# Kernel tuning notes

Measured on AMD Instinct MI355X. Metric: run time of the kernel, lower is better.

## Reference

```python
import jax, jax.numpy as jnp
import numpy as np

N_USER, N_ITEM = 100000, 50000
E = 500000
D, ED = 128, 16


def setup_inputs() -> dict:
    key = jax.random.key(0)
    ks = jax.random.split(key, 14)
    return {
        "h_user": jax.random.normal(ks[0], (N_USER, D), jnp.float32),
        "h_item": jax.random.normal(ks[1], (N_ITEM, D), jnp.float32),
        "ef_orders": jax.random.normal(ks[2], (E, ED), jnp.float32),
        "ef_rev": jax.random.normal(ks[3], (E, ED), jnp.float32),
        "W1": jax.random.normal(ks[4], (2 * D + ED, 128), jnp.float32) * 0.05,
        "b1": jax.random.normal(ks[5], (128,), jnp.float32) * 0.05,
        "W2": jax.random.normal(ks[6], (128, 32), jnp.float32) * 0.05,
        "b2": jax.random.normal(ks[7], (32,), jnp.float32) * 0.05,
        "W3": jax.random.normal(ks[8], (32, 1), jnp.float32) * 0.05,
        "b3": jax.random.normal(ks[9], (1,), jnp.float32) * 0.05,
        "src_orders": jax.random.randint(ks[10], (E,), 0, N_USER, jnp.int64),
        "dst_orders": jax.random.randint(ks[11], (E,), 0, N_ITEM, jnp.int64),
        "src_rev": jax.random.randint(ks[12], (E,), 0, N_ITEM, jnp.int64),
        "dst_rev": jax.random.randint(ks[13], (E,), 0, N_USER, jnp.int64),
    }


def _edge_mlp(h_src, h_dst, src, dst, ef, W1, b1, W2, b2, W3, b3):
    # gather per-edge endpoint embeddings, concat with edge features: [E, 2D+ED]
    x = jnp.concatenate([h_src[src], h_dst[dst], ef], axis=1)
    x = jax.nn.relu(x @ W1 + b1)   # [E, 128]
    x = jax.nn.relu(x @ W2 + b2)   # [E, 32]
    return jax.nn.sigmoid(x @ W3 + b3)  # [E, 1]


def reference(h_user, h_item, ef_orders, ef_rev, W1, b1, W2, b2, W3, b3,
              src_orders, dst_orders, src_rev, dst_rev):
    # etype (user, orders, item)
    out_orders = _edge_mlp(h_user, h_item, src_orders, dst_orders, ef_orders,
                           W1, b1, W2, b2, W3, b3)
    # etype (item, rev-orders, user)
    out_rev = _edge_mlp(h_item, h_user, src_rev, dst_rev, ef_rev,
                        W1, b1, W2, b2, W3, b3)
    return out_orders, out_rev
```

## Files before the change

kernel.cpp:

```cpp
#include <hip/hip_runtime.h>
#include <hip/hip_bf16.h>

typedef __attribute__((ext_vector_type(8))) short bfrag;
typedef __attribute__((ext_vector_type(4))) float facc;
typedef __attribute__((ext_vector_type(2))) float f32x2;

static __device__ __forceinline__ float bf2f_lo(unsigned int u) {
    return __uint_as_float(u << 16);
}
static __device__ __forceinline__ float bf2f_hi(unsigned int u) {
    return __uint_as_float(u & 0xffff0000u);
}
static __device__ __forceinline__ unsigned short f2bf(float f) {
    __hip_bfloat16 b = __float2bfloat16(f);
    return *reinterpret_cast<unsigned short*>(&b);
}

extern "C" __global__ __launch_bounds__(256)
void precompute_mfma(const float* __restrict__ hu, int nu,
                     const float* __restrict__ hi, int ni,
                     const float* __restrict__ W1,
                     unsigned char* __restrict__ Yu,
                     unsigned char* __restrict__ Yi)
{
    const int tid = threadIdx.x, wave = tid >> 6, lane = tid & 63;
    const int g = lane >> 4, e16 = lane & 15;
    const int c0 = wave * 64;

    bfrag bfr[4][4];
    #pragma unroll
    for (int nt = 0; nt < 4; ++nt) {
        const int j = c0 + nt * 16 + e16;
        #pragma unroll
        for (int kk = 0; kk < 4; ++kk) {
            bfrag v;
            #pragma unroll
            for (int i = 0; i < 8; ++i) {
                int k = kk * 32 + g * 8 + i;
                float w = (j < 128) ? W1[(size_t)k * 128 + j]
                                    : W1[(size_t)(128 + k) * 128 + (j - 128)];
                v[i] = (short)f2bf(w);
            }
            bfr[nt][kk] = v;
        }
    }

    const int tu = (nu + 15) >> 4, ti = (ni + 15) >> 4, tt = tu + ti;
    for (int tile = blockIdx.x; tile < tt; tile += gridDim.x) {
        const float* h; unsigned char* Y; int n, node0;
        if (tile < tu) { h = hu; Y = Yu; n = nu; node0 = tile * 16; }
        else           { h = hi; Y = Yi; n = ni; node0 = (tile - tu) * 16; }

        int arow = node0 + e16; if (arow >= n) arow = n - 1;
        facc acc[4] = {{0,0,0,0},{0,0,0,0},{0,0,0,0},{0,0,0,0}};
        #pragma unroll
        for (int kk = 0; kk < 4; ++kk) {
            const float* ap = h + (size_t)arow * 128 + kk * 32 + g * 8;
            float4 a0 = *(const float4*)ap;
            float4 a1v = *(const float4*)(ap + 4);
            bfrag af;
            af[0] = (short)f2bf(a0.x);  af[1] = (short)f2bf(a0.y);
            af[2] = (short)f2bf(a0.z);  af[3] = (short)f2bf(a0.w);
            af[4] = (short)f2bf(a1v.x); af[5] = (short)f2bf(a1v.y);
            af[6] = (short)f2bf(a1v.z); af[7] = (short)f2bf(a1v.w);
            #pragma unroll
            for (int nt = 0; nt < 4; ++nt)
                acc[nt] = __builtin_amdgcn_mfma_f32_16x16x32_bf16(af, bfr[nt][kk], acc[nt], 0, 0, 0);
        }
        #pragma unroll
        for (int nt = 0; nt < 4; ++nt) {
            unsigned int pk = __builtin_amdgcn_cvt_pk_fp8_f32(acc[nt][0], acc[nt][1], 0u, false);
            pk = __builtin_amdgcn_cvt_pk_fp8_f32(acc[nt][2], acc[nt][3], pk, true);
            #pragma unroll
            for (int r = 0; r < 4; ++r) {
                int row = node0 + g * 4 + r;
                if (row < n)
                    Y[(size_t)row * 256 + c0 + nt * 16 + e16] =
                        (unsigned char)(pk >> (8 * r));
            }
        }
    }
}

extern "C" __global__ __launch_bounds__(256, 3)
void edge_mfma(const unsigned char* __restrict__ Yu,
               const unsigned char* __restrict__ Yi,
               const float* __restrict__ ef_orders,
               const float* __restrict__ ef_rev,
               const int* __restrict__ src_orders,
               const int* __restrict__ dst_orders,
               const int* __restrict__ src_rev,
               const int* __restrict__ dst_rev,
               const float* __restrict__ W1,
               const float* __restrict__ b1,
               const float* __restrict__ W2,
               const float* __restrict__ b2,
               const float* __restrict__ W3,
               const float* __restrict__ b3,
               float* __restrict__ out, int E)
{
    __shared__ __align__(16) unsigned short d1_lds[4][16][128];
    const int tid = threadIdx.x, wave = tid >> 6, lane = tid & 63;
    const int g = lane >> 4, e16 = lane & 15;
    unsigned short (*my_lds)[128] = d1_lds[wave];
    const int swzb = (e16 & 7) << 3;

    bfrag a1[8];
    #pragma unroll
    for (int t = 0; t < 8; ++t) {
        bfrag v;
        #pragma unroll
        for (int i = 0; i < 8; ++i) {
            unsigned short s16 = 0;
            if (i < 4)                s16 = f2bf(W1[(size_t)(256 + 4 * g + i) * 128 + t * 16 + e16]);
            else if (i == 4 && g == 0) s16 = f2bf(b1[t * 16 + e16]);
            v[i] = (short)s16;
        }
        a1[t] = v;
    }
    bfrag w2t[2][4];
    #pragma unroll
    for (int nt = 0; nt < 2; ++nt)
        #pragma unroll
        for (int kk = 0; kk < 4; ++kk) {
            bfrag v;
            #pragma unroll
            for (int i = 0; i < 8; ++i) {
                int k = (kk >> 1) * 64 + 16 * g + (kk & 1) * 8 + i;
                v[i] = (short)f2bf(W2[(size_t)k * 32 + nt * 16 + e16]);
            }
            w2t[nt][kk] = v;
        }
    float b2v[2][4], w3v[2][4];
    #pragma unroll
    for (int nt = 0; nt < 2; ++nt)
        #pragma unroll
        for (int r = 0; r < 4; ++r) {
            b2v[nt][r] = b2[nt * 16 + g * 4 + r];
            w3v[nt][r] = W3[nt * 16 + g * 4 + r];
        }
    const float b3s = b3[0];

    const long twoE = 2L * E;
    const int nbatch = (int)((twoE + 15) >> 4);
    const int stride = gridDim.x * 4;
    int b = blockIdx.x * 4 + wave;

    int s_pf = 0, d_pf = 0;
    uint4 ysA, ysB, ydA, ydB;
    float4 efq = make_float4(0, 0, 0, 0);

#define LOADIDX(BB) do {                                                      \
        long el_ = ((long)(BB) << 4) + e16;                                   \
        if (el_ >= twoE) el_ = twoE - 1;                                      \
        const bool rv_ = el_ >= E;                                            \
        const int ee_ = (int)(rv_ ? el_ - E : el_);                           \
        s_pf = (rv_ ? src_rev : src_orders)[ee_];                             \
        d_pf = (rv_ ? dst_rev : dst_orders)[ee_];                             \
    } while (0)

#define GATHER(BB) do {                                                       \
        long el_ = ((long)(BB) << 4) + e16;                                   \
        if (el_ >= twoE) el_ = twoE - 1;                                      \
        const bool rv_ = el_ >= E;                                            \
        const int ee_ = (int)(rv_ ? el_ - E : el_);                           \
        const unsigned char* ps_ = (rv_ ? Yi : Yu) + (size_t)s_pf * 256 + g * 16; \
        const unsigned char* pd_ = (rv_ ? Yu : Yi) + (size_t)d_pf * 256 + 128 + g * 16; \
        ysA = *(const uint4*)(ps_);       ysB = *(const uint4*)(ps_ + 64);    \
        ydA = *(const uint4*)(pd_);       ydB = *(const uint4*)(pd_ + 64);    \
        efq = *(const float4*)((rv_ ? ef_rev : ef_orders) + (size_t)ee_ * 16 + g * 4); \
    } while (0)

#define PSTEP(KK, YSL, YSH, YDL, YDH) do {                                    \
        const int dlo_ = (((KK) >> 1) * 64 + 16 * g + ((KK) & 1) * 8) ^ swzb; \
        uint4 wv = *(const uint4*)&my_lds[e16][dlo_];                         \
        f32x2 s01 = __builtin_amdgcn_cvt_pk_f32_fp8(YSL, false);              \
        f32x2 s23 = __builtin_amdgcn_cvt_pk_f32_fp8(YSL, true);               \
        f32x2 s45 = __builtin_amdgcn_cvt_pk_f32_fp8(YSH, false);              \
        f32x2 s67 = __builtin_amdgcn_cvt_pk_f32_fp8(YSH, true);               \
        f32x2 d01 = __builtin_amdgcn_cvt_pk_f32_fp8(YDL, false);              \
        f32x2 d23 = __builtin_amdgcn_cvt_pk_f32_fp8(YDL, true);               \
        f32x2 d45 = __builtin_amdgcn_cvt_pk_f32_fp8(YDH, false);              \
        f32x2 d67 = __builtin_amdgcn_cvt_pk_f32_fp8(YDH, true);               \
        float p0 = s01[0] + d01[0] + bf2f_lo(wv.x);                           \
        float p1 = s01[1] + d01[1] + bf2f_hi(wv.x);                           \
        float p2 = s23[0] + d23[0] + bf2f_lo(wv.y);                           \
        float p3 = s23[1] + d23[1] + bf2f_hi(wv.y);                           \
        float p4 = s45[0] + d45[0] + bf2f_lo(wv.z);                           \
        float p5 = s45[1] + d45[1] + bf2f_hi(wv.z);                           \
        float p6 = s67[0] + d67[0] + bf2f_lo(wv.w);                           \
        float p7 = s67[1] + d67[1] + bf2f_hi(wv.w);                           \
        bfrag pa;                                                             \
        pa[0] = (short)f2bf(fmaxf(p0, 0.f)); pa[1] = (short)f2bf(fmaxf(p1, 0.f)); \
        pa[2] = (short)f2bf(fmaxf(p2, 0.f)); pa[3] = (short)f2bf(fmaxf(p3, 0.f)); \
        pa[4] = (short)f2bf(fmaxf(p4, 0.f)); pa[5] = (short)f2bf(fmaxf(p5, 0.f)); \
        pa[6] = (short)f2bf(fmaxf(p6, 0.f)); pa[7] = (short)f2bf(fmaxf(p7, 0.f)); \
        acc2a = __builtin_amdgcn_mfma_f32_16x16x32_bf16(w2t[0][KK], pa, acc2a, 0, 0, 0); \
        acc2b = __builtin_amdgcn_mfma_f32_16x16x32_bf16(w2t[1][KK], pa, acc2b, 0, 0, 0); \
    } while (0)

    if (b < nbatch) {
        LOADIDX(b);
        GATHER(b);
        if (b + stride < nbatch) LOADIDX(b + stride);
    }

    for (; b < nbatch; b += stride) {
        bfrag eb;
        #pragma unroll
        for (int i = 0; i < 8; ++i) eb[i] = 0;
        eb[0] = (short)f2bf(efq.x); eb[1] = (short)f2bf(efq.y);
        eb[2] = (short)f2bf(efq.z); eb[3] = (short)f2bf(efq.w);
        if (g == 0) eb[4] = (short)0x3F80;

        #pragma unroll
        for (int t = 0; t < 8; ++t) {
            facc zero = {0, 0, 0, 0};
            facc d1 = __builtin_amdgcn_mfma_f32_16x16x32_bf16(a1[t], eb, zero, 0, 0, 0);
            ushort4 u;
            u.x = f2bf(d1[0]); u.y = f2bf(d1[1]); u.z = f2bf(d1[2]); u.w = f2bf(d1[3]);
            *(ushort4*)&my_lds[e16][(t * 16 + g * 4) ^ swzb] = u;
        }

        facc acc2a = {0, 0, 0, 0}, acc2b = {0, 0, 0, 0};
        PSTEP(0, ysA.x, ysA.y, ydA.x, ydA.y);
        PSTEP(1, ysA.z, ysA.w, ydA.z, ydA.w);
        PSTEP(2, ysB.x, ysB.y, ydB.x, ydB.y);
        PSTEP(3, ysB.z, ysB.w, ydB.z, ydB.w);

        const int bn = b + stride;
        if (bn < nbatch) GATHER(bn);

        float h3 = 0.f;
        #pragma unroll
        for (int r = 0; r < 4; ++r) {
            float h2 = fmaxf(acc2a[r] + b2v[0][r], 0.f);
            h3 = fmaf(h2, w3v[0][r], h3);
        }
        #pragma unroll
        for (int r = 0; r < 4; ++r) {
            float h2 = fmaxf(acc2b[r] + b2v[1][r], 0.f);
            h3 = fmaf(h2, w3v[1][r], h3);
        }
        h3 += __shfl_xor(h3, 16, 64);
        h3 += __shfl_xor(h3, 32, 64);
        const long el = ((long)b << 4) + lane;
        if (lane < 16 && el < twoE)
            out[el] = 1.f / (1.f + __expf(-(h3 + b3s)));

        const int b2n = b + 2 * stride;
        if (b2n < nbatch) LOADIDX(b2n);
    }
#undef LOADIDX
#undef GATHER
#undef PSTEP
}

extern "C" __global__ __launch_bounds__(256)
void edge_mlp_direct(const float* __restrict__ h_user,
                     const float* __restrict__ h_item,
                     const float* __restrict__ ef_orders,
                     const float* __restrict__ ef_rev,
                     const int* __restrict__ src_orders,
                     const int* __restrict__ dst_orders,
                     const int* __restrict__ src_rev,
                     const int* __restrict__ dst_rev,
                     const float* __restrict__ W1,
                     const float* __restrict__ b1,
                     const float* __restrict__ W2,
                     const float* __restrict__ b2,
                     const float* __restrict__ W3,
                     const float* __restrict__ b3,
                     float* __restrict__ out, int E)
{
    __shared__ unsigned short W1s[256][128];
    __shared__ float xbuf[4][256];
    __shared__ float h1s[4][128];
    const int tid = threadIdx.x;
    const int wave = tid >> 6, lane = tid & 63;
    const int f0 = 2 * lane;
    const int j2 = lane & 31;
    const int kb = (lane >> 5) * 64;

    for (int i = tid; i < 256 * 128; i += 256)
        W1s[i >> 7][i & 127] = f2bf(W1[i]);
    __syncthreads();

    float w1c0[16], w1c1[16];
    #pragma unroll
    for (int k = 0; k < 16; ++k) {
        w1c0[k] = W1[(256 + k) * 128 + f0];
        w1c1[k] = W1[(256 + k) * 128 + f0 + 1];
    }
    float w2r[64];
    #pragma unroll
    for (int kk = 0; kk < 64; ++kk)
        w2r[kk] = W2[(kb + kk) * 32 + j2];
    const float b10 = b1[f0], b11 = b1[f0 + 1];
    const float b2vv = b2[j2], w3vv = W3[j2], b3v = b3[0];

    const long twoE = 2L * E;
    for (long e = (long)blockIdx.x * 4 + wave; e < twoE; e += (long)gridDim.x * 4) {
        const bool rv = (e >= E);
        const int ee = (int)(rv ? e - E : e);
        const int s = (rv ? src_rev : src_orders)[ee];
        const int d = (rv ? dst_rev : dst_orders)[ee];
        const float* hs = rv ? h_item : h_user;
        const float* hd = rv ? h_user : h_item;
        const float* efp = rv ? ef_rev : ef_orders;

        xbuf[wave][lane]       = hs[(size_t)s * 128 + lane];
        xbuf[wave][64 + lane]  = hs[(size_t)s * 128 + 64 + lane];
        xbuf[wave][128 + lane] = hd[(size_t)d * 128 + lane];
        xbuf[wave][192 + lane] = hd[(size_t)d * 128 + 64 + lane];
        __builtin_amdgcn_wave_barrier();

        float p0 = b10, p1 = b11;
        #pragma unroll 8
        for (int k = 0; k < 256; ++k) {
            float xv = xbuf[wave][k];
            unsigned int w = *(const unsigned int*)&W1s[k][f0];
            p0 = fmaf(xv, bf2f_lo(w), p0);
            p1 = fmaf(xv, bf2f_hi(w), p1);
        }
        const float efv = efp[(size_t)ee * 16 + (lane & 15)];
        #pragma unroll
        for (int k = 0; k < 16; ++k) {
            float ek = __shfl(efv, k, 64);
            p0 = fmaf(ek, w1c0[k], p0);
            p1 = fmaf(ek, w1c1[k], p1);
        }
        p0 = fmaxf(p0, 0.0f);
        p1 = fmaxf(p1, 0.0f);

        *(float2*)&h1s[wave][f0] = make_float2(p0, p1);
        __builtin_amdgcn_wave_barrier();
        float acc = 0.0f;
        #pragma unroll
        for (int q = 0; q < 16; ++q) {
            float4 hv = *(const float4*)&h1s[wave][kb + q * 4];
            acc = fmaf(hv.x, w2r[4 * q + 0], acc);
            acc = fmaf(hv.y, w2r[4 * q + 1], acc);
            acc = fmaf(hv.z, w2r[4 * q + 2], acc);
            acc = fmaf(hv.w, w2r[4 * q + 3], acc);
        }
        __builtin_amdgcn_wave_barrier();
        acc += __shfl_xor(acc, 32, 64);
        float h2 = fmaxf(acc + b2vv, 0.0f);
        float v = h2 * w3vv;
        v += __shfl_xor(v, 16, 64);
        v += __shfl_xor(v, 8, 64);
        v += __shfl_xor(v, 4, 64);
        v += __shfl_xor(v, 2, 64);
        v += __shfl_xor(v, 1, 64);
        if (lane == 0)
            out[e] = 1.0f / (1.0f + __expf(-(v + b3v)));
    }
}

extern "C" void kernel_launch(void* const* d_in, const int* in_sizes, int n_in,
                              void* d_out, int out_size, void* d_ws, size_t ws_size,
                              hipStream_t stream)
{
    const float* h_user    = (const float*)d_in[0];
    const float* h_item    = (const float*)d_in[1];
    const float* ef_orders = (const float*)d_in[2];
    const float* ef_rev    = (const float*)d_in[3];
    const float* W1        = (const float*)d_in[4];
    const float* b1        = (const float*)d_in[5];
    const float* W2        = (const float*)d_in[6];
    const float* b2        = (const float*)d_in[7];
    const float* W3        = (const float*)d_in[8];
    const float* b3        = (const float*)d_in[9];
    const int* src_orders  = (const int*)d_in[10];
    const int* dst_orders  = (const int*)d_in[11];
    const int* src_rev     = (const int*)d_in[12];
    const int* dst_rev     = (const int*)d_in[13];

    const int n_user = in_sizes[0] / 128;
    const int n_item = in_sizes[1] / 128;
    const int E      = in_sizes[2] / 16;
    float* out = (float*)d_out;

    const size_t need = (size_t)(n_user + n_item) * 256;
    if (ws_size >= need) {
        unsigned char* Yu = (unsigned char*)d_ws;
        unsigned char* Yi = Yu + (size_t)n_user * 256;
        precompute_mfma<<<2048, 256, 0, stream>>>(h_user, n_user, h_item, n_item, W1, Yu, Yi);
        edge_mfma<<<1024, 256, 0, stream>>>(Yu, Yi, ef_orders, ef_rev,
            src_orders, dst_orders, src_rev, dst_rev,
            W1, b1, W2, b2, W3, b3, out, E);
    } else {
        edge_mlp_direct<<<4096, 256, 0, stream>>>(h_user, h_item, ef_orders, ef_rev,
            src_orders, dst_orders, src_rev, dst_rev,
            W1, b1, W2, b2, W3, b3, out, E);
    }
}
```

Baseline: 125.3 us.

## Stage node embeddings through LDS with prefetch and swap MFMA operands for packed stores

In the precompute kernel, each block now loads the next 16-node tile of embeddings into registers while computing the current one, then stages it into a double-buffered LDS array. Previously each of the four waves re-read the same rows from global memory. The MFMA operands are swapped so the accumulator is transposed, and each lane writes four contiguous fp8 bytes as one 32-bit store instead of four scattered byte stores. The change adds two block barriers per tile and some LDS traffic.

```diff
diff --git a/kernel.cpp b/kernel.cpp
--- a/kernel.cpp
+++ b/kernel.cpp
@@ -23,11 +23,12 @@
                      unsigned char* __restrict__ Yu,
                      unsigned char* __restrict__ Yi)
 {
+    __shared__ __align__(16) float hstage[2][16][132];
     const int tid = threadIdx.x, wave = tid >> 6, lane = tid & 63;
     const int g = lane >> 4, e16 = lane & 15;
     const int c0 = wave * 64;
 
-    bfrag bfr[4][4];
+    bfrag aw1[4][4];
     #pragma unroll
     for (int nt = 0; nt < 4; ++nt) {
         const int j = c0 + nt * 16 + e16;
@@ -41,45 +42,89 @@
                                     : W1[(size_t)(128 + k) * 128 + (j - 128)];
                 v[i] = (short)f2bf(w);
             }
-            bfr[nt][kk] = v;
-        }
-    }
+            aw1[nt][kk] = v;
+        }
+    }
+
+    const int srow = tid >> 5;
+    const int scol = (tid & 31) * 4;
 
     const int tu = (nu + 15) >> 4, ti = (ni + 15) >> 4, tt = tu + ti;
-    for (int tile = blockIdx.x; tile < tt; tile += gridDim.x) {
-        const float* h; unsigned char* Y; int n, node0;
-        if (tile < tu) { h = hu; Y = Yu; n = nu; node0 = tile * 16; }
-        else           { h = hi; Y = Yi; n = ni; node0 = (tile - tu) * 16; }
-
-        int arow = node0 + e16; if (arow >= n) arow = n - 1;
+    const int stride = gridDim.x;
+    int tile = blockIdx.x;
+
+    const float* hs_c = hu; unsigned char* Y_c = Yu; int n_c = nu, node0_c = 0;
+    const float* hs_n; unsigned char* Y_n; int n_n, node0_n;
+    float4 sA, sB;
+
+#define SETSRC(T, HS, YP, NN, N0) do {                                        \
+        if ((T) < tu) { HS = hu; YP = Yu; NN = nu; N0 = (T) * 16; }           \
+        else          { HS = hi; YP = Yi; NN = ni; N0 = ((T) - tu) * 16; }    \
+    } while (0)
+
+#define LOADTILE(HS, NN, N0) do {                                             \
+        int rA_ = (N0) + srow;     if (rA_ >= (NN)) rA_ = (NN) - 1;           \
+        int rB_ = (N0) + 8 + srow; if (rB_ >= (NN)) rB_ = (NN) - 1;           \
+        sA = *(const float4*)((HS) + (size_t)rA_ * 128 + scol);               \
+        sB = *(const float4*)((HS) + (size_t)rB_ * 128 + scol);               \
+    } while (0)
+
+#define STAGE(BUF) do {                                                       \
+        *(float4*)&hstage[BUF][srow][scol]     = sA;                          \
+        *(float4*)&hstage[BUF][8 + srow][scol] = sB;                          \
+    } while (0)
+
+    if (tile < tt) {
+        SETSRC(tile, hs_c, Y_c, n_c, node0_c);
+        LOADTILE(hs_c, n_c, node0_c);
+        STAGE(0);
+    }
+    __syncthreads();
+    int buf = 0;
+
+    for (; tile < tt; tile += stride) {
+        const int tn = tile + stride;
+        if (tn < tt) {
+            SETSRC(tn, hs_n, Y_n, n_n, node0_n);
+            LOADTILE(hs_n, n_n, node0_n);
+        }
+
         facc acc[4] = {{0,0,0,0},{0,0,0,0},{0,0,0,0},{0,0,0,0}};
         #pragma unroll
         for (int kk = 0; kk < 4; ++kk) {
-            const float* ap = h + (size_t)arow * 128 + kk * 32 + g * 8;
-            float4 a0 = *(const float4*)ap;
-            float4 a1v = *(const float4*)(ap + 4);
-            bfrag af;
-            af[0] = (short)f2bf(a0.x);  af[1] = (short)f2bf(a0.y);
-            af[2] = (short)f2bf(a0.z);  af[3] = (short)f2bf(a0.w);
-            af[4] = (short)f2bf(a1v.x); af[5] = (short)f2bf(a1v.y);
-            af[6] = (short)f2bf(a1v.z); af[7] = (short)f2bf(a1v.w);
+            const float4 b0 = *(const float4*)&hstage[buf][e16][kk * 32 + g * 8];
+            const float4 b1 = *(const float4*)&hstage[buf][e16][kk * 32 + g * 8 + 4];
+            bfrag bf;
+            bf[0] = (short)f2bf(b0.x); bf[1] = (short)f2bf(b0.y);
+            bf[2] = (short)f2bf(b0.z); bf[3] = (short)f2bf(b0.w);
+            bf[4] = (short)f2bf(b1.x); bf[5] = (short)f2bf(b1.y);
+            bf[6] = (short)f2bf(b1.z); bf[7] = (short)f2bf(b1.w);
             #pragma unroll
             for (int nt = 0; nt < 4; ++nt)
-                acc[nt] = __builtin_amdgcn_mfma_f32_16x16x32_bf16(af, bfr[nt][kk], acc[nt], 0, 0, 0);
-        }
-        #pragma unroll
-        for (int nt = 0; nt < 4; ++nt) {
-            unsigned int pk = __builtin_amdgcn_cvt_pk_fp8_f32(acc[nt][0], acc[nt][1], 0u, false);
-            pk = __builtin_amdgcn_cvt_pk_fp8_f32(acc[nt][2], acc[nt][3], pk, true);
+                acc[nt] = __builtin_amdgcn_mfma_f32_16x16x32_bf16(aw1[nt][kk], bf, acc[nt], 0, 0, 0);
+        }
+
+        const int node = node0_c + e16;
+        if (node < n_c) {
             #pragma unroll
-            for (int r = 0; r < 4; ++r) {
-                int row = node0 + g * 4 + r;
-                if (row < n)
-                    Y[(size_t)row * 256 + c0 + nt * 16 + e16] =
-                        (unsigned char)(pk >> (8 * r));
+            for (int nt = 0; nt < 4; ++nt) {
+                unsigned int pk = __builtin_amdgcn_cvt_pk_fp8_f32(acc[nt][0], acc[nt][1], 0u, false);
+                pk = __builtin_amdgcn_cvt_pk_fp8_f32(acc[nt][2], acc[nt][3], pk, true);
+                *(unsigned int*)&Y_c[(size_t)node * 256 + c0 + nt * 16 + g * 4] = pk;
             }
         }
-    }
+
+        if (tn < tt) {
+            __syncthreads();
+            STAGE(buf ^ 1);
+            __syncthreads();
+            hs_c = hs_n; Y_c = Y_n; n_c = n_n; node0_c = node0_n;
+        }
+        buf ^= 1;
+    }
+#undef SETSRC
+#undef LOADTILE
+#undef STAGE
 }
 
 extern "C" __global__ __launch_bounds__(256, 3)
```

Result: faster. 112.9 us (-9.9%).
